# Performance work log

Hardware: AMD Instinct MI355X
Metric: run time of the kernel (lower is better)

Reference implementation:

```python
import jax, jax.numpy as jnp
import numpy as np

# ---- config (matches init_kwargs) ----
B, NP, DIM, HEADS, DH, NDIM = 32, 576, 512, 8, 64, 16
N = NP + 1                 # seq len incl cls token = 577
INNER = HEADS * DH         # 512


def setup_inputs() -> dict:
    key = jax.random.key(0)
    ks = jax.random.split(key, 11)
    D2 = 2 * DIM  # bidirectional EMA doubles kernel dim
    return {
        "x": jax.random.normal(ks[0], (B, N, DIM), jnp.float32),
        "W_qk": jax.random.normal(ks[1], (DIM, 2 * INNER), jnp.float32) / np.float32(np.sqrt(DIM)),
        "W_v": jax.random.normal(ks[2], (DIM, INNER), jnp.float32) / np.float32(np.sqrt(DIM)),
        "W_out": jax.random.normal(ks[3], (INNER, DIM), jnp.float32) / np.float32(np.sqrt(INNER)),
        "b_out": jnp.zeros((DIM,), jnp.float32),
        "rel_bias": jax.random.normal(ks[4], (2 * N - 1,), jnp.float32) * 0.02,
        "ema_delta": jax.random.normal(ks[5], (D2, NDIM, 1), jnp.float32),
        "ema_alpha": jax.random.normal(ks[6], (D2, NDIM, 1), jnp.float32),
        "ema_beta": jax.random.normal(ks[7], (D2, NDIM, 1), jnp.float32) * 0.5,
        "ema_gamma": jax.random.normal(ks[8], (D2, NDIM), jnp.float32) * 0.5,
        "ema_omega": jax.random.normal(ks[9], (DIM,), jnp.float32),
    }


def _ema_move(x, delta, alpha, beta, gamma, omega):
    """Bidirectional MultiHeadEMA (MEGA) via FFT convolution. x: (B, L, D)."""
    b, L, d = x.shape
    scale = jnp.asarray(np.sqrt(1.0 / NDIM), x.dtype)
    p = jax.nn.sigmoid(delta)                      # (2D, N, 1)
    q = 1.0 - p * jax.nn.sigmoid(alpha)            # (2D, N, 1), in (0,1)
    vander = jnp.arange(L, dtype=x.dtype)[None, None, :] * jnp.log(q)  # (2D, N, L)
    kern = (p * beta) * jnp.exp(vander)            # (2D, N, L)
    k = jnp.einsum('dnl,dn->dl', kern, gamma * scale)  # (2D, L)
    k1, k2 = k[:d], k[d:]
    # combined bidirectional kernel, length 2L-1
    kk = jnp.pad(k1, ((0, 0), (L - 1, 0))) + jnp.pad(k2[:, ::-1], ((0, 0), (0, L - 1)))
    xt = jnp.pad(x.transpose(0, 2, 1), ((0, 0), (0, 0), (L - 1, 0)))  # (B, D, 2L-1)
    fft_len = 2 * L - 1
    nfft = 2 * fft_len
    out = jnp.fft.irfft(jnp.fft.rfft(xt, n=nfft) * jnp.fft.rfft(kk, n=nfft)[None], n=nfft)
    s = 2 * L - 2
    out = out[..., s:s + L].transpose(0, 2, 1).astype(x.dtype)  # (B, L, D)
    return jax.nn.silu(out + x * omega)


def _rel_pos_bias(rb, seq_len):
    """RelativePositionalBias (MEGA): (2*N-1,) param -> (seq_len, seq_len) bias."""
    max_pos = N
    bvec = rb[max_pos - seq_len: max_pos + seq_len - 1]   # (2*seq_len-1,)
    t = jnp.pad(bvec, (0, seq_len))
    t = jnp.tile(t, seq_len)[:-seq_len].reshape(seq_len, 3 * seq_len - 2)
    r = (2 * seq_len - 1) // 2
    return t[:, r:t.shape[1] - r]


def reference(x, W_qk, W_v, W_out, b_out, rel_bias,
              ema_delta, ema_alpha, ema_beta, ema_gamma, ema_omega):
    b, n, _ = x.shape
    cls_tok = x[:, :1]
    moved = _ema_move(x[:, 1:], ema_delta, ema_alpha, ema_beta, ema_gamma, ema_omega)
    xm = jnp.concatenate([cls_tok, moved], axis=1)        # (B, N, DIM)
    q, k = jnp.split(xm @ W_qk, 2, axis=-1)
    v = xm @ W_v                                          # smooth_v_as_well=True

    def heads(t):
        return t.reshape(b, n, HEADS, DH).transpose(0, 2, 1, 3)  # (B, H, N, DH)

    q, k, v = heads(q), heads(k), heads(v)
    dots = jnp.einsum('bhid,bhjd->bhij', q, k) * (DH ** -0.5)
    attn = jax.nn.softmax(dots, axis=-1)
    attn = attn + _rel_pos_bias(rel_bias, n)[None, None]  # bias added AFTER softmax
    out = jnp.einsum('bhij,bhjd->bhid', attn, v)
    out = out.transpose(0, 2, 1, 3).reshape(b, n, INNER)
    return out @ W_out + b_out
```

## Files before the change

### kernel.cpp

```cpp
#include <hip/hip_runtime.h>

typedef unsigned short ushort;

typedef __bf16 bf16x8 __attribute__((ext_vector_type(8)));
typedef float  f32x4  __attribute__((ext_vector_type(4)));
typedef unsigned short u16x8 __attribute__((ext_vector_type(8)));
typedef unsigned short u16x4 __attribute__((ext_vector_type(4)));
typedef unsigned int   u32x2 __attribute__((ext_vector_type(2)));

static constexpr int BB   = 32;
static constexpr int NN   = 577;
static constexpr int LL   = 576;
static constexpr int DIMC = 512;
static constexpr int BN   = BB * NN;

static constexpr size_t SZ_WQKVT = 1536ull * 512 * 2;
static constexpr size_t SZ_WOUTT = 512ull * 512 * 2;
static constexpr size_t SZ_QK    = (size_t)BN * 1024 * 2;
static constexpr size_t SZ_V     = (size_t)BN * 512 * 2;
static constexpr size_t SZ_VT    = 256ull * 64 * 640 * 2;
static constexpr size_t OFF_WQKVT = 0;
static constexpr size_t OFF_WOUTT = OFF_WQKVT + SZ_WQKVT;
static constexpr size_t OFF_QTAB  = OFF_WOUTT + SZ_WOUTT;
static constexpr size_t OFF_CTAB  = OFF_QTAB + 65536;
static constexpr size_t OFF_QK    = OFF_CTAB + 65536;
static constexpr size_t OFF_V     = OFF_QK + SZ_QK;
static constexpr size_t OFF_REGION= OFF_V + SZ_V;
static constexpr size_t OFF_XM    = OFF_REGION;
static constexpr size_t OFF_VT    = OFF_REGION;
static constexpr size_t OFF_AO    = OFF_REGION + SZ_VT;
static constexpr size_t OFF_ST    = OFF_AO;
static constexpr size_t WS_NEEDED = OFF_AO + SZ_V;

__device__ __forceinline__ ushort bf16bits(float f) {
  unsigned int u = __builtin_bit_cast(unsigned int, f);
  u = (u + 0x7fffu + ((u >> 16) & 1u)) >> 16;
  return (ushort)u;
}
__device__ __forceinline__ unsigned int bf16pk(float lo, float hi) {
  unsigned int u0 = __builtin_bit_cast(unsigned int, lo);
  unsigned int u1 = __builtin_bit_cast(unsigned int, hi);
  unsigned int a0 = u0 + 0x7fffu + ((u0 >> 16) & 1u);
  unsigned int a1 = u1 + 0x7fffu + ((u1 >> 16) & 1u);
  return __builtin_amdgcn_perm(a1, a0, 0x07060302);
}
__device__ __forceinline__ float sigmoidf_(float z) { return 1.f / (1.f + __expf(-z)); }
__device__ __forceinline__ float siluf(float z)     { return z / (1.f + __expf(-z)); }
__device__ __forceinline__ void gload16(const ushort* g, ushort* l) {
  __builtin_amdgcn_global_load_lds(
      (const __attribute__((address_space(1))) unsigned int*)g,
      (__attribute__((address_space(3))) unsigned int*)l, 16, 0, 0);
}

__global__ __launch_bounds__(256) void k_prep(
    const float* __restrict__ delta, const float* __restrict__ alpha,
    const float* __restrict__ beta,  const float* __restrict__ gamma,
    const float* __restrict__ Wqk,   const float* __restrict__ Wv,
    const float* __restrict__ Wout,
    float* __restrict__ qtab, float* __restrict__ ctab,
    ushort* __restrict__ Wqkvt, ushort* __restrict__ Woutt)
{
  int idx = blockIdx.x * 256 + threadIdx.x;
  if (idx < 16384) {
    float p = sigmoidf_(delta[idx]);
    float q = 1.f - p * sigmoidf_(alpha[idx]);
    qtab[idx] = q;
    ctab[idx] = p * beta[idx] * gamma[idx] * 0.25f;
  }
  int i2 = idx - 16384;
  if (i2 >= 0 && i2 < 1536 * 512) {
    int n = i2 >> 9, k = i2 & 511;
    float w = (n < 1024) ? Wqk[k * 1024 + n] : Wv[k * 512 + (n - 1024)];
    Wqkvt[i2] = bf16bits(w);
  }
  int i3 = i2 - 1536 * 512;
  if (i3 >= 0 && i3 < 512 * 512) {
    int n = i3 >> 9, k = i3 & 511;
    Woutt[i3] = bf16bits(Wout[k * 512 + n]);
  }
}


__global__ __launch_bounds__(64) void k_ema_p1(
    const float* __restrict__ x, const float* __restrict__ qtab,
    float* __restrict__ st)
{
  const int gx = blockIdx.x, cy = blockIdx.y, b = blockIdx.z;
  if (gx < 8) {
    const int d = gx * 64 + threadIdx.x;
    float q[16], h[16];
    #pragma unroll
    for (int n = 0; n < 16; ++n) { q[n] = qtab[d*16+n]; h[n] = 0.f; }
    const float* xp = x + ((size_t)b * NN + 1) * DIMC + d;
    const int blo = cy * 9;
    float xn[8];
    #pragma unroll
    for (int u = 0; u < 8; ++u) xn[u] = xp[(blo * 8 + u) * DIMC];
    for (int blk = blo; blk < blo + 9; ++blk) {
      float xv[8];
      #pragma unroll
      for (int u = 0; u < 8; ++u) xv[u] = xn[u];
      if (blk < blo + 8) {
        #pragma unroll
        for (int u = 0; u < 8; ++u) xn[u] = xp[((blk + 1) * 8 + u) * DIMC];
      }
      #pragma unroll
      for (int u = 0; u < 8; ++u) {
        float xx = xv[u];
        #pragma unroll
        for (int n = 0; n < 16; ++n) h[n] = fmaf(q[n], h[n], xx);
      }
    }
    float* sp = st + (((size_t)b * 8 + cy) * 16) * 512 + d;
    #pragma unroll
    for (int n = 0; n < 16; ++n) sp[n * 512] = h[n];
  } else {
    const int d = (gx - 8) * 64 + threadIdx.x;
    float q[16], g[16];
    #pragma unroll
    for (int n = 0; n < 16; ++n) { q[n] = qtab[(d+512)*16+n]; g[n] = 0.f; }
    const float* xp = x + ((size_t)b * NN + 1) * DIMC + d;
    const int blo = (7 - cy) * 9;
    float xn[8];
    #pragma unroll
    for (int u = 0; u < 8; ++u) xn[u] = xp[((blo + 8) * 8 + u) * DIMC];
    for (int blk = blo + 8; blk >= blo; --blk) {
      float xv[8];
      #pragma unroll
      for (int u = 0; u < 8; ++u) xv[u] = xn[u];
      if (blk > blo) {
        #pragma unroll
        for (int u = 0; u < 8; ++u) xn[u] = xp[((blk - 1) * 8 + u) * DIMC];
      }
      #pragma unroll
      for (int u = 7; u >= 0; --u) {
        float xx = xv[u];
        #pragma unroll
        for (int n = 0; n < 16; ++n) g[n] = fmaf(q[n], g[n], xx);
      }
    }
    float* sp = st + (((size_t)(32 + b) * 8 + cy) * 16) * 512 + d;
    #pragma unroll
    for (int n = 0; n < 16; ++n) sp[n * 512] = g[n];
  }
}

__global__ __launch_bounds__(256) void k_ema_mid(
    const float* __restrict__ qtab, float* __restrict__ st)
{
  int idx = blockIdx.x * 256 + threadIdx.x;
  int d = idx & 511;
  int rest = idx >> 9;
  int n = rest & 15;
  int db = rest >> 4;
  int dir = db >> 5;
  float q = qtab[(((size_t)dir << 9) + d) * 16 + n];
  float q2 = q * q, q4 = q2 * q2, q8 = q4 * q4;
  float q16 = q8 * q8, q32 = q16 * q16, q64 = q32 * q32;
  float qL = q64 * q8;
  float h = 0.f;
  float* sp = st + ((size_t)db * 128 + n) * 512 + d;
  #pragma unroll
  for (int c = 0; c < 8; ++c) {
    float tmp = (c < 7) ? sp[c * 8192] : 0.f;
    sp[c * 8192] = h;
    h = fmaf(qL, h, tmp);
  }
}

__global__ __launch_bounds__(64) void k_ema_fuse(
    const float* __restrict__ x, const float* __restrict__ qtab,
    const float* __restrict__ ctab, const float* __restrict__ st,
    const float* __restrict__ omega, ushort* __restrict__ xm)
{
  __shared__ _Float16 yb[72 * 64];
  const int lane = threadIdx.x;
  const int gx = blockIdx.x, cy = blockIdx.y, b = blockIdx.z;
  const int d = gx * 64 + lane;
  const float* xp = x + ((size_t)b * NN + 1 + cy * 72) * DIMC + d;
  {
    float q[16], c[16], g[16];
    const float* sp = st + (((size_t)(32 + b) * 8 + (7 - cy)) * 16) * 512 + d;
    #pragma unroll
    for (int n = 0; n < 16; ++n) {
      q[n] = qtab[(d + 512) * 16 + n];
      c[n] = ctab[(d + 512) * 16 + n];
      g[n] = sp[n * 512];
    }
    float xn[8];
    #pragma unroll
    for (int u = 0; u < 8; ++u) xn[u] = xp[(64 + u) * DIMC];
    for (int blk = 8; blk >= 0; --blk) {
      float xv[8];
      #pragma unroll
      for (int u = 0; u < 8; ++u) xv[u] = xn[u];
      if (blk > 0) {
        #pragma unroll
        for (int u = 0; u < 8; ++u) xn[u] = xp[((blk - 1) * 8 + u) * DIMC];
      }
      #pragma unroll
      for (int u = 7; u >= 0; --u) {
        float xx = xv[u], y = 0.f;
        #pragma unroll
        for (int n = 0; n < 16; ++n) { g[n] = fmaf(q[n], g[n], xx); y = fmaf(c[n], g[n], y); }
        yb[(blk * 8 + u) * 64 + lane] = (_Float16)y;
      }
    }
  }
  __syncthreads();
  {
    float q[16], c[16], h[16];
    const float* sp = st + (((size_t)b * 8 + cy) * 16) * 512 + d;
    #pragma unroll
    for (int n = 0; n < 16; ++n) {
      q[n] = qtab[d * 16 + n];
      c[n] = ctab[d * 16 + n];
      h[n] = sp[n * 512];
    }
    const float om = omega[d];
    ushort* op = xm + ((size_t)b * NN + 1 + cy * 72) * DIMC + d;
    float xn[8];
    #pragma unroll
    for (int u = 0; u < 8; ++u) xn[u] = xp[u * DIMC];
    for (int blk = 0; blk < 9; ++blk) {
      float xv[8];
      #pragma unroll
      for (int u = 0; u < 8; ++u) xv[u] = xn[u];
      if (blk < 8) {
        #pragma unroll
        for (int u = 0; u < 8; ++u) xn[u] = xp[((blk + 1) * 8 + u) * DIMC];
      }
      #pragma unroll
      for (int u = 0; u < 8; ++u) {
        float xx = xv[u], y = 0.f;
        #pragma unroll
        for (int n = 0; n < 16; ++n) { h[n] = fmaf(q[n], h[n], xx); y = fmaf(c[n], h[n], y); }
        float s = y + (float)yb[(blk * 8 + u) * 64 + lane] + xx * om;
        op[(blk * 8 + u) * DIMC] = bf16bits(siluf(s));
      }
    }
  }
  if (cy == 0) {
    size_t e0 = ((size_t)b * NN) * DIMC + d;
    xm[e0] = bf16bits(x[e0]);
  }
}

__global__ __launch_bounds__(256) void k_qkv(
    const ushort* __restrict__ A, const ushort* __restrict__ Bt,
    ushort* __restrict__ qk, ushort* __restrict__ v)
{
  __shared__ alignas(16) ushort lA[128 * 32];
  __shared__ alignas(16) ushort lB[128 * 32];
  const int tid = threadIdx.x, wv = tid >> 6, lane = tid & 63;
  const int quad = lane >> 4, c16 = lane & 15;
  const int fid = blockIdx.y * 12 + blockIdx.x;
  const int xcd = fid & 7, ord = fid >> 3;
  const int wg  = (xcd < 4 ? xcd * 218 : 872 + (xcd - 4) * 217) + ord;
  const int row0 = (wg / 12) * 128, n0 = (wg % 12) * 128;
  const int wm = (wv >> 1) * 64, wn = (wv & 1) * 64;
  const int sr  = wv * 32 + (lane >> 2);
  const int scs = ((lane & 3) ^ (sr & 3)) * 8;
  int ga[2], gb[2];
  #pragma unroll
  for (int s = 0; s < 2; ++s) {
    int r = row0 + sr + s * 16; if (r > BN - 1) r = BN - 1;
    ga[s] = r;
    gb[s] = n0 + sr + s * 16;
  }
  const int xread = (quad ^ (c16 & 3)) * 8;
  f32x4 z4 = {0.f, 0.f, 0.f, 0.f};
  f32x4 acc[4][4];
  #pragma unroll
  for (int mi = 0; mi < 4; ++mi)
    #pragma unroll
    for (int ni = 0; ni < 4; ++ni) acc[mi][ni] = z4;

  for (int kt = 0; kt < 16; ++kt) {
    const int k0 = kt * 32;
    __syncthreads();
    #pragma unroll
    for (int s = 0; s < 2; ++s) {
      gload16(A  + (size_t)ga[s] * 512 + k0 + scs, lA + (wv * 32 + s * 16) * 32);
      gload16(Bt + (size_t)gb[s] * 512 + k0 + scs, lB + (wv * 32 + s * 16) * 32);
    }
    __syncthreads();
    bf16x8 af[4], bfv[4];
    #pragma unroll
    for (int mi = 0; mi < 4; ++mi)
      af[mi] = *(const bf16x8*)(lA + (wm + mi * 16 + c16) * 32 + xread);
    #pragma unroll
    for (int ni = 0; ni < 4; ++ni)
      bfv[ni] = *(const bf16x8*)(lB + (wn + ni * 16 + c16) * 32 + xread);
    #pragma unroll
    for (int mi = 0; mi < 4; ++mi)
      #pragma unroll
      for (int ni = 0; ni < 4; ++ni)
        acc[mi][ni] = __builtin_amdgcn_mfma_f32_16x16x32_bf16(af[mi], bfv[ni], acc[mi][ni], 0, 0, 0);
  }
  const bool isv = (n0 >= 1024);
  const float osc = (n0 < 512) ? 0.1803368801111f : 1.0f;
  #pragma unroll
  for (int mi = 0; mi < 4; ++mi) {
    #pragma unroll
    for (int r = 0; r < 4; ++r) {
      int grow = row0 + wm + mi * 16 + quad * 4 + r;
      if (grow < BN) {
        #pragma unroll
        for (int ni = 0; ni < 4; ++ni) {
          int col = n0 + wn + ni * 16 + c16;
          ushort vb = bf16bits(acc[mi][ni][r] * osc);
          if (!isv) qk[(size_t)grow * 1024 + col] = vb;
          else      v[(size_t)grow * 512 + (col - 1024)] = vb;
        }
      }
    }
  }
}

__global__ __launch_bounds__(256) void k_vtrans(
    const ushort* __restrict__ v, ushort* __restrict__ vt)
{
  __shared__ alignas(16) ushort lt[64 * 72];
  const int tid = threadIdx.x;
  const int bh = blockIdx.y, b = bh >> 3, h = bh & 7;
  const int j0 = blockIdx.x * 64;
  #pragma unroll
  for (int pass = 0; pass < 2; ++pass) {
    int cch = pass * 256 + tid;
    int jl = cch >> 3, cc = cch & 7;
    int gj = j0 + jl;
    u16x8 val = {0, 0, 0, 0, 0, 0, 0, 0};
    if (gj < 577) val = *(const u16x8*)(v + ((size_t)(b * NN + gj)) * 512 + h * 64 + cc * 8);
    *(u16x8*)(lt + jl * 72 + cc * 8) = val;
  }
  __syncthreads();
  #pragma unroll
  for (int pass = 0; pass < 2; ++pass) {
    int cch = pass * 256 + tid;
    int dh = cch >> 3, jc = cch & 7;
    u16x8 o;
    #pragma unroll
    for (int e = 0; e < 8; ++e) o[e] = lt[(jc * 8 + e) * 72 + dh];
    *(u16x8*)(vt + ((size_t)(bh * 64 + dh)) * 640 + j0 + jc * 8) = o;
  }
}

__global__ __launch_bounds__(256) void k_fattn(
    const ushort* __restrict__ qk, const ushort* __restrict__ vt,
    const float* __restrict__ relb, ushort* __restrict__ ao)
{
  __shared__ alignas(16) ushort lk[64 * 64];
  __shared__ alignas(16) ushort lv[64 * 64];
  __shared__ alignas(16) ushort lp[128 * 64];
  __shared__ ushort lbias16[1280];
  const int tid = threadIdx.x, wv = tid >> 6, lane = tid & 63;
  const int quad = lane >> 4, c16 = lane & 15;
  const int bh = blockIdx.x, b = bh >> 3, h = bh & 7;
  const int i0 = blockIdx.y * 128, wm = wv * 32;
  for (int t = tid; t < 1280; t += 256) {
    int idx = t - 64;
    lbias16[t] = (idx >= 0 && idx < 1153) ? bf16bits(relb[idx]) : (ushort)0;
  }
  bf16x8 aq[2][2];
  #pragma unroll
  for (int ms = 0; ms < 2; ++ms) {
    int gi = i0 + wm + ms * 16 + c16; if (gi > 576) gi = 576;
    const ushort* qp = qk + ((size_t)(b * NN + gi)) * 1024 + h * 64;
    #pragma unroll
    for (int kk = 0; kk < 2; ++kk)
      aq[ms][kk] = *(const bf16x8*)(qp + (kk * 4 + quad) * 8);
  }
  const int s_r = tid >> 3, s_c = tid & 7;
  const ushort* kbase = qk + ((size_t)b * NN) * 1024 + 512 + h * 64 + s_c * 8;
  const ushort* vbase = vt + ((size_t)bh * 64) * 640 + s_c * 8;

  float lsum[2] = {0.f, 0.f};
  f32x4 z4 = {0.f, 0.f, 0.f, 0.f};
  f32x4 accp[2][4], accb[2][4];
  #pragma unroll
  for (int ms = 0; ms < 2; ++ms)
    #pragma unroll
    for (int ns = 0; ns < 4; ++ns) { accp[ms][ns] = z4; accb[ms][ns] = z4; }

  u16x8 sk[2], sv[2];
  #pragma unroll
  for (int it = 0; it < 2; ++it) {
    int r = it * 32 + s_r;
    sk[it] = *(const u16x8*)(kbase + (size_t)r * 1024);
    sv[it] = *(const u16x8*)(vbase + (size_t)r * 640);
  }

  for (int jt = 0; jt < 10; ++jt) {
    __syncthreads();
    #pragma unroll
    for (int it = 0; it < 2; ++it) {
      int r = it * 32 + s_r;
      int pc = (s_c ^ (r & 7)) * 8;
      *(u16x8*)(lk + r * 64 + pc) = sk[it];
      *(u16x8*)(lv + r * 64 + pc) = sv[it];
    }
    __syncthreads();
    if (jt < 9) {
      const int j0n = (jt + 1) * 64;
      #pragma unroll
      for (int it = 0; it < 2; ++it) {
        int r = it * 32 + s_r;
        int gj = j0n + r; if (gj > 576) gj = 576;
        sk[it] = *(const u16x8*)(kbase + (size_t)gj * 1024);
        sv[it] = *(const u16x8*)(vbase + (size_t)r * 640 + j0n);
      }
    }
    #pragma unroll
    for (int ms = 0; ms < 2; ++ms) {
      f32x4 dacc[4] = {z4, z4, z4, z4};
      #pragma unroll
      for (int kk = 0; kk < 2; ++kk) {
        const int ck = kk * 4 + quad;
        #pragma unroll
        for (int ns = 0; ns < 4; ++ns) {
          const int row = ns * 16 + c16;
          bf16x8 bk = *(const bf16x8*)(lk + row * 64 + ((ck ^ (row & 7)) * 8));
          dacc[ns] = __builtin_amdgcn_mfma_f32_16x16x32_bf16(bk, aq[ms][kk], dacc[ns], 0, 0, 0);
        }
      }
      const int irow = wm + ms * 16 + c16;
      const int xr = irow & 7;
      #pragma unroll
      for (int ns = 0; ns < 4; ++ns) {
        float ex[4];
        #pragma unroll
        for (int r = 0; r < 4; ++r) {
          float e = __builtin_amdgcn_exp2f(dacc[ns][r]);
          if (jt == 9 && (ns * 16 + quad * 4 + r) >= 1) e = 0.f;
          ex[r] = e;
        }
        lsum[ms] += (ex[0] + ex[1]) + (ex[2] + ex[3]);
        u32x2 pw = { bf16pk(ex[0], ex[1]), bf16pk(ex[2], ex[3]) };
        const int lc = ns * 2 + (quad >> 1);
        *(u32x2*)(lp + irow * 64 + ((lc ^ xr) * 8) + (quad & 1) * 4) = pw;
      }
    }
    const int j0 = jt * 64;
    #pragma unroll
    for (int kk = 0; kk < 2; ++kk) {
      const int ck = kk * 4 + quad;
      bf16x8 ap[2], ab[2];
      #pragma unroll
      for (int ms = 0; ms < 2; ++ms) {
        const int row = wm + ms * 16 + c16;
        ap[ms] = *(const bf16x8*)(lp + row * 64 + ((ck ^ (row & 7)) * 8));
        u16x8 abu;
        const int base = 64 + 576 + j0 + kk * 32 + quad * 8 - (i0 + row);
        #pragma unroll
        for (int e = 0; e < 8; ++e) abu[e] = lbias16[base + e];
        ab[ms] = __builtin_bit_cast(bf16x8, abu);
      }
      #pragma unroll
      for (int ns = 0; ns < 4; ++ns) {
        const int row = ns * 16 + c16;
        bf16x8 bV = *(const bf16x8*)(lv + row * 64 + ((ck ^ (row & 7)) * 8));
        #pragma unroll
        for (int ms = 0; ms < 2; ++ms) {
          accp[ms][ns] = __builtin_amdgcn_mfma_f32_16x16x32_bf16(ap[ms], bV, accp[ms][ns], 0, 0, 0);
          accb[ms][ns] = __builtin_amdgcn_mfma_f32_16x16x32_bf16(ab[ms], bV, accb[ms][ns], 0, 0, 0);
        }
      }
    }
  }
  float tot[2];
  #pragma unroll
  for (int ms = 0; ms < 2; ++ms) {
    float t = lsum[ms];
    t += __shfl_xor(t, 16);
    t += __shfl_xor(t, 32);
    tot[ms] = t;
  }
  #pragma unroll
  for (int ms = 0; ms < 2; ++ms) {
    #pragma unroll
    for (int r = 0; r < 4; ++r) {
      float li = 1.f / __shfl(tot[ms], quad * 4 + r);
      int ii = i0 + wm + ms * 16 + quad * 4 + r;
      if (ii < 577) {
        #pragma unroll
        for (int ns = 0; ns < 4; ++ns)
          ao[((size_t)(b * NN + ii)) * 512 + h * 64 + ns * 16 + c16] =
              bf16bits(accp[ms][ns][r] * li + accb[ms][ns][r]);
      }
    }
  }
}

__global__ __launch_bounds__(256) void k_out(
    const ushort* __restrict__ A, const ushort* __restrict__ Bt,
    const float* __restrict__ bout, float* __restrict__ out)
{
  __shared__ alignas(16) ushort lA[128 * 32];
  __shared__ alignas(16) ushort lB[128 * 32];
  const int tid = threadIdx.x, wv = tid >> 6, lane = tid & 63;
  const int quad = lane >> 4, c16 = lane & 15;
  const int row0 = blockIdx.y * 128, n0 = blockIdx.x * 128;
  const int wm = (wv >> 1) * 64, wn = (wv & 1) * 64;
  const int sr  = wv * 32 + (lane >> 2);
  const int scs = ((lane & 3) ^ (sr & 3)) * 8;
  int ga[2], gb[2];
  #pragma unroll
  for (int s = 0; s < 2; ++s) {
    int r = row0 + sr + s * 16; if (r > BN - 1) r = BN - 1;
    ga[s] = r;
    gb[s] = n0 + sr + s * 16;
  }
  const int xread = (quad ^ (c16 & 3)) * 8;
  f32x4 z4 = {0.f, 0.f, 0.f, 0.f};
  f32x4 acc[4][4];
  #pragma unroll
  for (int mi = 0; mi < 4; ++mi)
    #pragma unroll
    for (int ni = 0; ni < 4; ++ni) acc[mi][ni] = z4;

  for (int kt = 0; kt < 16; ++kt) {
    const int k0 = kt * 32;
    __syncthreads();
    #pragma unroll
    for (int s = 0; s < 2; ++s) {
      gload16(A  + (size_t)ga[s] * 512 + k0 + scs, lA + (wv * 32 + s * 16) * 32);
      gload16(Bt + (size_t)gb[s] * 512 + k0 + scs, lB + (wv * 32 + s * 16) * 32);
    }
    __syncthreads();
    bf16x8 af[4], bfv[4];
    #pragma unroll
    for (int mi = 0; mi < 4; ++mi)
      af[mi] = *(const bf16x8*)(lA + (wm + mi * 16 + c16) * 32 + xread);
    #pragma unroll
    for (int ni = 0; ni < 4; ++ni)
      bfv[ni] = *(const bf16x8*)(lB + (wn + ni * 16 + c16) * 32 + xread);
    #pragma unroll
    for (int mi = 0; mi < 4; ++mi)
      #pragma unroll
      for (int ni = 0; ni < 4; ++ni)
        acc[mi][ni] = __builtin_amdgcn_mfma_f32_16x16x32_bf16(af[mi], bfv[ni], acc[mi][ni], 0, 0, 0);
  }
  #pragma unroll
  for (int mi = 0; mi < 4; ++mi) {
    #pragma unroll
    for (int r = 0; r < 4; ++r) {
      int grow = row0 + wm + mi * 16 + quad * 4 + r;
      if (grow < BN) {
        #pragma unroll
        for (int ni = 0; ni < 4; ++ni) {
          int col = n0 + wn + ni * 16 + c16;
          out[(size_t)grow * 512 + col] = acc[mi][ni][r] + bout[col];
        }
      }
    }
  }
}

extern "C" void kernel_launch(void* const* d_in, const int* in_sizes, int n_in,
                              void* d_out, int out_size, void* d_ws, size_t ws_size,
                              hipStream_t stream) {
  (void)in_sizes; (void)n_in; (void)out_size;
  if (ws_size < WS_NEEDED) return;
  const float* x    = (const float*)d_in[0];
  const float* Wqk  = (const float*)d_in[1];
  const float* Wv   = (const float*)d_in[2];
  const float* Wout = (const float*)d_in[3];
  const float* bout = (const float*)d_in[4];
  const float* relb = (const float*)d_in[5];
  const float* edel = (const float*)d_in[6];
  const float* ealp = (const float*)d_in[7];
  const float* ebet = (const float*)d_in[8];
  const float* egam = (const float*)d_in[9];
  const float* eome = (const float*)d_in[10];

  char* ws = (char*)d_ws;
  ushort* Wqkvt = (ushort*)(ws + OFF_WQKVT);
  ushort* Woutt = (ushort*)(ws + OFF_WOUTT);
  float*  qtab  = (float*)(ws + OFF_QTAB);
  float*  ctab  = (float*)(ws + OFF_CTAB);
  ushort* qkb   = (ushort*)(ws + OFF_QK);
  ushort* vb    = (ushort*)(ws + OFF_V);
  ushort* xm    = (ushort*)(ws + OFF_XM);
  ushort* vtb   = (ushort*)(ws + OFF_VT);
  ushort* aob   = (ushort*)(ws + OFF_AO);
  float*  stf   = (float*)(ws + OFF_ST);
  float*  outp  = (float*)d_out;

  k_prep<<<dim3(4160), dim3(256), 0, stream>>>(edel, ealp, ebet, egam, Wqk, Wv, Wout,
                                               qtab, ctab, Wqkvt, Woutt);
  k_ema_p1<<<dim3(16, 7, 32), dim3(64), 0, stream>>>(x, qtab, stf);
  k_ema_mid<<<dim3(2048), dim3(256), 0, stream>>>(qtab, stf);
  k_ema_fuse<<<dim3(8, 8, 32), dim3(64), 0, stream>>>(x, qtab, ctab, stf, eome, xm);
  k_qkv<<<dim3(12, 145), dim3(256), 0, stream>>>(xm, Wqkvt, qkb, vb);
  k_vtrans<<<dim3(10, 256), dim3(256), 0, stream>>>(vb, vtb);
  k_fattn<<<dim3(256, 5), dim3(256), 0, stream>>>(qkb, vtb, relb, aob);
  k_out<<<dim3(4, 145), dim3(256), 0, stream>>>(aob, Woutt, bout, outp);
}
```

Baseline: 299.8 us.

## Use packed FP32 FMAs in EMA scans and halve attention query tile

The EMA scan kernels now hold their 16 state lanes as 8 float2 vectors and update them with elementwise vector FMAs, so the compiler can emit packed FP32 instructions (v_pk_fma_f32) and halve the FMA instruction count. The flash-attention kernel drops from 128 to 64 query rows per block, one 16-row MFMA tile per wave, and launches twice as many blocks. This aims to cut register and LDS pressure and raise occupancy. The cost is that each block reloads its K/V tiles for half as many queries, doubling K/V traffic into LDS.

```diff
diff --git a/kernel.cpp b/kernel.cpp
--- a/kernel.cpp
+++ b/kernel.cpp
@@ -4,6 +4,7 @@
 
 typedef __bf16 bf16x8 __attribute__((ext_vector_type(8)));
 typedef float  f32x4  __attribute__((ext_vector_type(4)));
+typedef float  f32x2  __attribute__((ext_vector_type(2)));
 typedef unsigned short u16x8 __attribute__((ext_vector_type(8)));
 typedef unsigned short u16x4 __attribute__((ext_vector_type(4)));
 typedef unsigned int   u32x2 __attribute__((ext_vector_type(2)));
@@ -88,9 +89,12 @@
   const int gx = blockIdx.x, cy = blockIdx.y, b = blockIdx.z;
   if (gx < 8) {
     const int d = gx * 64 + threadIdx.x;
-    float q[16], h[16];
-    #pragma unroll
-    for (int n = 0; n < 16; ++n) { q[n] = qtab[d*16+n]; h[n] = 0.f; }
+    f32x2 q[8], h[8];
+    #pragma unroll
+    for (int n = 0; n < 8; ++n) {
+      q[n] = *(const f32x2*)(qtab + d * 16 + 2 * n);
+      h[n] = (f32x2){0.f, 0.f};
+    }
     const float* xp = x + ((size_t)b * NN + 1) * DIMC + d;
     const int blo = cy * 9;
     float xn[8];
@@ -106,19 +110,22 @@
       }
       #pragma unroll
       for (int u = 0; u < 8; ++u) {
-        float xx = xv[u];
-        #pragma unroll
-        for (int n = 0; n < 16; ++n) h[n] = fmaf(q[n], h[n], xx);
+        f32x2 x2 = {xv[u], xv[u]};
+        #pragma unroll
+        for (int n = 0; n < 8; ++n) h[n] = __builtin_elementwise_fma(q[n], h[n], x2);
       }
     }
     float* sp = st + (((size_t)b * 8 + cy) * 16) * 512 + d;
     #pragma unroll
-    for (int n = 0; n < 16; ++n) sp[n * 512] = h[n];
+    for (int n = 0; n < 8; ++n) { sp[(2*n) * 512] = h[n][0]; sp[(2*n+1) * 512] = h[n][1]; }
   } else {
     const int d = (gx - 8) * 64 + threadIdx.x;
-    float q[16], g[16];
-    #pragma unroll
-    for (int n = 0; n < 16; ++n) { q[n] = qtab[(d+512)*16+n]; g[n] = 0.f; }
+    f32x2 q[8], g[8];
+    #pragma unroll
+    for (int n = 0; n < 8; ++n) {
+      q[n] = *(const f32x2*)(qtab + (d + 512) * 16 + 2 * n);
+      g[n] = (f32x2){0.f, 0.f};
+    }
     const float* xp = x + ((size_t)b * NN + 1) * DIMC + d;
     const int blo = (7 - cy) * 9;
     float xn[8];
@@ -134,14 +141,14 @@
       }
       #pragma unroll
       for (int u = 7; u >= 0; --u) {
-        float xx = xv[u];
-        #pragma unroll
-        for (int n = 0; n < 16; ++n) g[n] = fmaf(q[n], g[n], xx);
+        f32x2 x2 = {xv[u], xv[u]};
+        #pragma unroll
+        for (int n = 0; n < 8; ++n) g[n] = __builtin_elementwise_fma(q[n], g[n], x2);
       }
     }
     float* sp = st + (((size_t)(32 + b) * 8 + cy) * 16) * 512 + d;
     #pragma unroll
-    for (int n = 0; n < 16; ++n) sp[n * 512] = g[n];
+    for (int n = 0; n < 8; ++n) { sp[(2*n) * 512] = g[n][0]; sp[(2*n+1) * 512] = g[n][1]; }
   }
 }
 
@@ -179,13 +186,13 @@
   const int d = gx * 64 + lane;
   const float* xp = x + ((size_t)b * NN + 1 + cy * 72) * DIMC + d;
   {
-    float q[16], c[16], g[16];
+    f32x2 q[8], c[8], g[8];
     const float* sp = st + (((size_t)(32 + b) * 8 + (7 - cy)) * 16) * 512 + d;
     #pragma unroll
-    for (int n = 0; n < 16; ++n) {
-      q[n] = qtab[(d + 512) * 16 + n];
-      c[n] = ctab[(d + 512) * 16 + n];
-      g[n] = sp[n * 512];
+    for (int n = 0; n < 8; ++n) {
+      q[n] = *(const f32x2*)(qtab + (d + 512) * 16 + 2 * n);
+      c[n] = *(const f32x2*)(ctab + (d + 512) * 16 + 2 * n);
+      g[n] = (f32x2){sp[(2*n) * 512], sp[(2*n+1) * 512]};
     }
     float xn[8];
     #pragma unroll
@@ -200,22 +207,26 @@
       }
       #pragma unroll
       for (int u = 7; u >= 0; --u) {
-        float xx = xv[u], y = 0.f;
-        #pragma unroll
-        for (int n = 0; n < 16; ++n) { g[n] = fmaf(q[n], g[n], xx); y = fmaf(c[n], g[n], y); }
-        yb[(blk * 8 + u) * 64 + lane] = (_Float16)y;
+        f32x2 x2 = {xv[u], xv[u]};
+        f32x2 yv = {0.f, 0.f};
+        #pragma unroll
+        for (int n = 0; n < 8; ++n) {
+          g[n] = __builtin_elementwise_fma(q[n], g[n], x2);
+          yv   = __builtin_elementwise_fma(c[n], g[n], yv);
+        }
+        yb[(blk * 8 + u) * 64 + lane] = (_Float16)(yv[0] + yv[1]);
       }
     }
   }
   __syncthreads();
   {
-    float q[16], c[16], h[16];
+    f32x2 q[8], c[8], h[8];
     const float* sp = st + (((size_t)b * 8 + cy) * 16) * 512 + d;
     #pragma unroll
-    for (int n = 0; n < 16; ++n) {
-      q[n] = qtab[d * 16 + n];
-      c[n] = ctab[d * 16 + n];
-      h[n] = sp[n * 512];
+    for (int n = 0; n < 8; ++n) {
+      q[n] = *(const f32x2*)(qtab + d * 16 + 2 * n);
+      c[n] = *(const f32x2*)(ctab + d * 16 + 2 * n);
+      h[n] = (f32x2){sp[(2*n) * 512], sp[(2*n+1) * 512]};
     }
     const float om = omega[d];
     ushort* op = xm + ((size_t)b * NN + 1 + cy * 72) * DIMC + d;
@@ -232,10 +243,14 @@
       }
       #pragma unroll
       for (int u = 0; u < 8; ++u) {
-        float xx = xv[u], y = 0.f;
-        #pragma unroll
-        for (int n = 0; n < 16; ++n) { h[n] = fmaf(q[n], h[n], xx); y = fmaf(c[n], h[n], y); }
-        float s = y + (float)yb[(blk * 8 + u) * 64 + lane] + xx * om;
+        f32x2 x2 = {xv[u], xv[u]};
+        f32x2 yv = {0.f, 0.f};
+        #pragma unroll
+        for (int n = 0; n < 8; ++n) {
+          h[n] = __builtin_elementwise_fma(q[n], h[n], x2);
+          yv   = __builtin_elementwise_fma(c[n], h[n], yv);
+        }
+        float s = (yv[0] + yv[1]) + (float)yb[(blk * 8 + u) * 64 + lane] + xv[u] * om;
         op[(blk * 8 + u) * DIMC] = bf16bits(siluf(s));
       }
     }
@@ -352,36 +367,33 @@
 {
   __shared__ alignas(16) ushort lk[64 * 64];
   __shared__ alignas(16) ushort lv[64 * 64];
-  __shared__ alignas(16) ushort lp[128 * 64];
+  __shared__ alignas(16) ushort lp[64 * 64];
   __shared__ ushort lbias16[1280];
   const int tid = threadIdx.x, wv = tid >> 6, lane = tid & 63;
   const int quad = lane >> 4, c16 = lane & 15;
   const int bh = blockIdx.x, b = bh >> 3, h = bh & 7;
-  const int i0 = blockIdx.y * 128, wm = wv * 32;
+  const int i0 = blockIdx.y * 64, wm = wv * 16;
   for (int t = tid; t < 1280; t += 256) {
     int idx = t - 64;
     lbias16[t] = (idx >= 0 && idx < 1153) ? bf16bits(relb[idx]) : (ushort)0;
   }
-  bf16x8 aq[2][2];
-  #pragma unroll
-  for (int ms = 0; ms < 2; ++ms) {
-    int gi = i0 + wm + ms * 16 + c16; if (gi > 576) gi = 576;
+  bf16x8 aq[2];
+  {
+    int gi = i0 + wm + c16; if (gi > 576) gi = 576;
     const ushort* qp = qk + ((size_t)(b * NN + gi)) * 1024 + h * 64;
     #pragma unroll
     for (int kk = 0; kk < 2; ++kk)
-      aq[ms][kk] = *(const bf16x8*)(qp + (kk * 4 + quad) * 8);
+      aq[kk] = *(const bf16x8*)(qp + (kk * 4 + quad) * 8);
   }
   const int s_r = tid >> 3, s_c = tid & 7;
   const ushort* kbase = qk + ((size_t)b * NN) * 1024 + 512 + h * 64 + s_c * 8;
   const ushort* vbase = vt + ((size_t)bh * 64) * 640 + s_c * 8;
 
-  float lsum[2] = {0.f, 0.f};
+  float lsum = 0.f;
   f32x4 z4 = {0.f, 0.f, 0.f, 0.f};
-  f32x4 accp[2][4], accb[2][4];
-  #pragma unroll
-  for (int ms = 0; ms < 2; ++ms)
-    #pragma unroll
-    for (int ns = 0; ns < 4; ++ns) { accp[ms][ns] = z4; accb[ms][ns] = z4; }
+  f32x4 accp[4], accb[4];
+  #pragma unroll
+  for (int ns = 0; ns < 4; ++ns) { accp[ns] = z4; accb[ns] = z4; }
 
   u16x8 sk[2], sv[2];
   #pragma unroll
@@ -411,20 +423,19 @@
         sv[it] = *(const u16x8*)(vbase + (size_t)r * 640 + j0n);
       }
     }
-    #pragma unroll
-    for (int ms = 0; ms < 2; ++ms) {
-      f32x4 dacc[4] = {z4, z4, z4, z4};
-      #pragma unroll
-      for (int kk = 0; kk < 2; ++kk) {
-        const int ck = kk * 4 + quad;
-        #pragma unroll
-        for (int ns = 0; ns < 4; ++ns) {
-          const int row = ns * 16 + c16;
-          bf16x8 bk = *(const bf16x8*)(lk + row * 64 + ((ck ^ (row & 7)) * 8));
-          dacc[ns] = __builtin_amdgcn_mfma_f32_16x16x32_bf16(bk, aq[ms][kk], dacc[ns], 0, 0, 0);
-        }
-      }
-      const int irow = wm + ms * 16 + c16;
+    f32x4 dacc[4] = {z4, z4, z4, z4};
+    #pragma unroll
+    for (int kk = 0; kk < 2; ++kk) {
+      const int ck = kk * 4 + quad;
+      #pragma unroll
+      for (int ns = 0; ns < 4; ++ns) {
+        const int row = ns * 16 + c16;
+        bf16x8 bk = *(const bf16x8*)(lk + row * 64 + ((ck ^ (row & 7)) * 8));
+        dacc[ns] = __builtin_amdgcn_mfma_f32_16x16x32_bf16(bk, aq[kk], dacc[ns], 0, 0, 0);
+      }
+    }
+    {
+      const int irow = wm + c16;
       const int xr = irow & 7;
       #pragma unroll
       for (int ns = 0; ns < 4; ++ns) {
@@ -435,7 +446,7 @@
           if (jt == 9 && (ns * 16 + quad * 4 + r) >= 1) e = 0.f;
           ex[r] = e;
         }
-        lsum[ms] += (ex[0] + ex[1]) + (ex[2] + ex[3]);
+        lsum += (ex[0] + ex[1]) + (ex[2] + ex[3]);
         u32x2 pw = { bf16pk(ex[0], ex[1]), bf16pk(ex[2], ex[3]) };
         const int lc = ns * 2 + (quad >> 1);
         *(u32x2*)(lp + irow * 64 + ((lc ^ xr) * 8) + (quad & 1) * 4) = pw;
@@ -445,49 +456,34 @@
     #pragma unroll
     for (int kk = 0; kk < 2; ++kk) {
       const int ck = kk * 4 + quad;
-      bf16x8 ap[2], ab[2];
-      #pragma unroll
-      for (int ms = 0; ms < 2; ++ms) {
-        const int row = wm + ms * 16 + c16;
-        ap[ms] = *(const bf16x8*)(lp + row * 64 + ((ck ^ (row & 7)) * 8));
-        u16x8 abu;
-        const int base = 64 + 576 + j0 + kk * 32 + quad * 8 - (i0 + row);
-        #pragma unroll
-        for (int e = 0; e < 8; ++e) abu[e] = lbias16[base + e];
-        ab[ms] = __builtin_bit_cast(bf16x8, abu);
-      }
+      const int row = wm + c16;
+      bf16x8 ap = *(const bf16x8*)(lp + row * 64 + ((ck ^ (row & 7)) * 8));
+      u16x8 abu;
+      const int base = 64 + 576 + j0 + kk * 32 + quad * 8 - (i0 + row);
+      #pragma unroll
+      for (int e = 0; e < 8; ++e) abu[e] = lbias16[base + e];
+      bf16x8 ab = __builtin_bit_cast(bf16x8, abu);
       #pragma unroll
       for (int ns = 0; ns < 4; ++ns) {
-        const int row = ns * 16 + c16;
-        bf16x8 bV = *(const bf16x8*)(lv + row * 64 + ((ck ^ (row & 7)) * 8));
-        #pragma unroll
-        for (int ms = 0; ms < 2; ++ms) {
-          accp[ms][ns] = __builtin_amdgcn_mfma_f32_16x16x32_bf16(ap[ms], bV, accp[ms][ns], 0, 0, 0);
-          accb[ms][ns] = __builtin_amdgcn_mfma_f32_16x16x32_bf16(ab[ms], bV, accb[ms][ns], 0, 0, 0);
-        }
-      }
-    }
-  }
-  float tot[2];
-  #pragma unroll
-  for (int ms = 0; ms < 2; ++ms) {
-    float t = lsum[ms];
-    t += __shfl_xor(t, 16);
-    t += __shfl_xor(t, 32);
-    tot[ms] = t;
-  }
-  #pragma unroll
-  for (int ms = 0; ms < 2; ++ms) {
-    #pragma unroll
-    for (int r = 0; r < 4; ++r) {
-      float li = 1.f / __shfl(tot[ms], quad * 4 + r);
-      int ii = i0 + wm + ms * 16 + quad * 4 + r;
-      if (ii < 577) {
-        #pragma unroll
-        for (int ns = 0; ns < 4; ++ns)
-          ao[((size_t)(b * NN + ii)) * 512 + h * 64 + ns * 16 + c16] =
-              bf16bits(accp[ms][ns][r] * li + accb[ms][ns][r]);
-      }
+        const int vrow = ns * 16 + c16;
+        bf16x8 bV = *(const bf16x8*)(lv + vrow * 64 + ((ck ^ (vrow & 7)) * 8));
+        accp[ns] = __builtin_amdgcn_mfma_f32_16x16x32_bf16(ap, bV, accp[ns], 0, 0, 0);
+        accb[ns] = __builtin_amdgcn_mfma_f32_16x16x32_bf16(ab, bV, accb[ns], 0, 0, 0);
+      }
+    }
+  }
+  float tot = lsum;
+  tot += __shfl_xor(tot, 16);
+  tot += __shfl_xor(tot, 32);
+  #pragma unroll
+  for (int r = 0; r < 4; ++r) {
+    float li = 1.f / __shfl(tot, quad * 4 + r);
+    int ii = i0 + wm + quad * 4 + r;
+    if (ii < 577) {
+      #pragma unroll
+      for (int ns = 0; ns < 4; ++ns)
+        ao[((size_t)(b * NN + ii)) * 512 + h * 64 + ns * 16 + c16] =
+            bf16bits(accp[ns][r] * li + accb[ns][r]);
     }
   }
 }
@@ -594,6 +590,6 @@
   k_ema_fuse<<<dim3(8, 8, 32), dim3(64), 0, stream>>>(x, qtab, ctab, stf, eome, xm);
   k_qkv<<<dim3(12, 145), dim3(256), 0, stream>>>(xm, Wqkvt, qkb, vb);
   k_vtrans<<<dim3(10, 256), dim3(256), 0, stream>>>(vb, vtb);
-  k_fattn<<<dim3(256, 5), dim3(256), 0, stream>>>(qkb, vtb, relb, aob);
+  k_fattn<<<dim3(256, 10), dim3(256), 0, stream>>>(qkb, vtb, relb, aob);
   k_out<<<dim3(4, 145), dim3(256), 0, stream>>>(aob, Woutt, bout, outp);
 }
```

Measured after the change: 307.6 us. +2.6%, slower.
